# Performance work log

Hardware: AMD Instinct MI355X
Metric: run time of the kernel (lower is better)

The kernel has to match this reference:

```python
import jax, jax.numpy as jnp
import numpy as np

B, S, D, H, F = 8, 1024, 1024, 16, 4096
DH = D // H  # 64
EPS = 1e-12


def _layer_norm(x, g, b):
    mu = jnp.mean(x, axis=-1, keepdims=True)
    var = jnp.mean(jnp.square(x - mu), axis=-1, keepdims=True)
    return (x - mu) / jnp.sqrt(var + EPS) * g + b


def setup_inputs() -> dict:
    key = jax.random.key(0)
    ks = jax.random.split(key, 16)
    sd = 0.02
    inp = {
        "x": jax.random.normal(ks[0], (B, S, D), dtype=jnp.float32),
        "attn_mask": jnp.ones((B, S), dtype=jnp.int32),
        # attention projections (torch Linear: W is [out, in])
        "Wq": jax.random.normal(ks[1], (D, D), dtype=jnp.float32) * sd,
        "bq": jnp.zeros((D,), dtype=jnp.float32),
        "Wk": jax.random.normal(ks[2], (D, D), dtype=jnp.float32) * sd,
        "bk": jnp.zeros((D,), dtype=jnp.float32),
        "Wv": jax.random.normal(ks[3], (D, D), dtype=jnp.float32) * sd,
        "bv": jnp.zeros((D,), dtype=jnp.float32),
        "Wo": jax.random.normal(ks[4], (D, D), dtype=jnp.float32) * sd,
        "bo": jnp.zeros((D,), dtype=jnp.float32),
        # sa_layer_norm
        "ln1_g": jnp.ones((D,), dtype=jnp.float32),
        "ln1_b": jnp.zeros((D,), dtype=jnp.float32),
        # FFN
        "W1": jax.random.normal(ks[5], (F, D), dtype=jnp.float32) * sd,
        "b1": jnp.zeros((F,), dtype=jnp.float32),
        "W2": jax.random.normal(ks[6], (D, F), dtype=jnp.float32) * sd,
        "b2": jnp.zeros((D,), dtype=jnp.float32),
        # output_layer_norm
        "ln2_g": jnp.ones((D,), dtype=jnp.float32),
        "ln2_b": jnp.zeros((D,), dtype=jnp.float32),
    }
    return inp


def reference(x, attn_mask, Wq, bq, Wk, bk, Wv, bv, Wo, bo,
              ln1_g, ln1_b, W1, b1, W2, b2, ln2_g, ln2_b):
    b, s, d = x.shape

    def proj_heads(inp, W, bias):
        y = jnp.einsum('bsd,ed->bse', inp, W) + bias  # torch Linear: x @ W.T + b
        return y.reshape(b, s, H, DH).transpose(0, 2, 1, 3)  # (b, h, s, dh)

    q = proj_heads(x, Wq, bq) / jnp.sqrt(jnp.float32(DH))
    k = proj_heads(x, Wk, bk)
    v = proj_heads(x, Wv, bv)

    scores = jnp.einsum('bhqe,bhke->bhqk', q, k)  # (b, h, s, s)
    pad = (attn_mask == 0)[:, None, None, :]      # (b, 1, 1, s)
    scores = jnp.where(pad, -jnp.inf, scores)
    weights = jax.nn.softmax(scores, axis=-1)

    ctx = jnp.einsum('bhqk,bhke->bhqe', weights, v)
    ctx = ctx.transpose(0, 2, 1, 3).reshape(b, s, d)
    sa_out = jnp.einsum('bsd,ed->bse', ctx, Wo) + bo

    h = _layer_norm(sa_out + x, ln1_g, ln1_b)

    ff = jnp.einsum('bsd,fd->bsf', h, W1) + b1
    ff = jax.nn.gelu(ff, approximate=False)
    ff = jnp.einsum('bsf,df->bsd', ff, W2) + b2

    out = _layer_norm(ff + h, ln2_g, ln2_b)
    return out
```

## Files before the change

kernel.cpp:

```cpp
#include <hip/hip_runtime.h>
#include <math.h>

typedef __attribute__((ext_vector_type(8))) short short8;
typedef __attribute__((ext_vector_type(4))) float f32x4;

__device__ __forceinline__ unsigned short f2bf(float f) {
  unsigned int u = __float_as_uint(f);
  u += 0x7fffu + ((u >> 16) & 1u);
  return (unsigned short)(u >> 16);
}

__device__ __forceinline__ float gelu_f(float v) {
  float xa = fabsf(v) * 0.70710678118f;
  float t = __builtin_amdgcn_rcpf(1.f + 0.3275911f * xa);
  float p = t * (0.254829592f +
            t * (-0.284496736f +
            t * (1.421413741f +
            t * (-1.453152027f + t * 1.061405429f))));
  float erfa = 1.f - p * __expf(-xa * xa);
  return 0.5f * v * (1.f + copysignf(erfa, v));
}

__device__ __forceinline__ void gll16(const unsigned short* g, unsigned short* l) {
  __builtin_amdgcn_global_load_lds(
      (const __attribute__((address_space(1))) unsigned int*)(uintptr_t)g,
      (__attribute__((address_space(3))) unsigned int*)(uintptr_t)l, 16, 0, 0);
}

__global__ __launch_bounds__(256) void cvt_f32_bf16(const float* __restrict__ in,
                                                    unsigned short* __restrict__ out,
                                                    int n4) {
  int i = blockIdx.x * 256 + threadIdx.x;
  if (i >= n4) return;
  float4 f = reinterpret_cast<const float4*>(in)[i];
  ushort4 o;
  o.x = f2bf(f.x); o.y = f2bf(f.y); o.z = f2bf(f.z); o.w = f2bf(f.w);
  reinterpret_cast<ushort4*>(out)[i] = o;
}

__global__ __launch_bounds__(256) void cvt4_f32_bf16(
    const float* __restrict__ a, const float* __restrict__ b,
    const float* __restrict__ c, const float* __restrict__ d,
    unsigned short* __restrict__ oa, unsigned short* __restrict__ ob,
    unsigned short* __restrict__ oc, unsigned short* __restrict__ od) {
  const float* in = (blockIdx.y == 0) ? a : (blockIdx.y == 1) ? b : (blockIdx.y == 2) ? c : d;
  unsigned short* out = (blockIdx.y == 0) ? oa : (blockIdx.y == 1) ? ob : (blockIdx.y == 2) ? oc : od;
  int i = blockIdx.x * 256 + threadIdx.x;
  float4 f = reinterpret_cast<const float4*>(in)[i];
  ushort4 o;
  o.x = f2bf(f.x); o.y = f2bf(f.y); o.z = f2bf(f.z); o.w = f2bf(f.w);
  reinterpret_cast<ushort4*>(out)[i] = o;
}

template <int EPI, bool SWAP>
__global__ __launch_bounds__(256) void gemm_nt(
    const unsigned short* __restrict__ A, const unsigned short* __restrict__ B,
    const float* __restrict__ bias, const float* __restrict__ bias_k,
    int K, int N, const float* __restrict__ resid,
    unsigned short* __restrict__ outb, float* __restrict__ outf) {
  __shared__ __align__(16) unsigned short As[2][128 * 32];
  __shared__ __align__(16) unsigned short Bs[2][128 * 32];
  const int t = threadIdx.x;
  const int tm = blockIdx.y * 128, tn = blockIdx.x * 128;
  const int lane = t & 63, wv = t >> 6;
  const int wr = wv >> 1, wc = wv & 1;
  const int l15 = lane & 15, quad = lane >> 4;
  const int srow = lane >> 2;
  const int scol = (lane & 3) << 3;

  const unsigned short* pa0 = &A[(size_t)(tm + wv * 32 + srow) * K + scol];
  const unsigned short* pa1 = &A[(size_t)(tm + wv * 32 + 16 + srow) * K + scol];
  const unsigned short* pb0 = &B[(size_t)(tn + wv * 32 + srow) * K + scol];
  const unsigned short* pb1 = &B[(size_t)(tn + wv * 32 + 16 + srow) * K + scol];
  unsigned short* la0 = &As[0][(wv * 2) * 512];
  unsigned short* la1 = &As[0][(wv * 2 + 1) * 512];
  unsigned short* lb0 = &Bs[0][(wv * 2) * 512];
  unsigned short* lb1 = &Bs[0][(wv * 2 + 1) * 512];

  const f32x4 zero = {0.f, 0.f, 0.f, 0.f};
  f32x4 acc[4][4];
#pragma unroll
  for (int i = 0; i < 4; ++i)
#pragma unroll
    for (int j = 0; j < 4; ++j) acc[i][j] = zero;

  gll16(pa0, la0); pa0 += 32;
  gll16(pa1, la1); pa1 += 32;
  gll16(pb0, lb0); pb0 += 32;
  gll16(pb1, lb1); pb1 += 32;

  const int nIter = K >> 5;
  for (int it = 0; it < nIter; ++it) {
    __syncthreads();
    const int cur = (it & 1) * 4096;
    const int nxt = 4096 - cur;
    if (it + 1 < nIter) {
      gll16(pa0, la0 + nxt); pa0 += 32;
      gll16(pa1, la1 + nxt); pa1 += 32;
      gll16(pb0, lb0 + nxt); pb0 += 32;
      gll16(pb1, lb1 + nxt); pb1 += 32;
    }
    short8 af[4], bfr[4];
#pragma unroll
    for (int i = 0; i < 4; ++i) {
      af[i] = *reinterpret_cast<const short8*>(&As[0][cur + (wr * 64 + i * 16 + l15) * 32 + quad * 8]);
      bfr[i] = *reinterpret_cast<const short8*>(&Bs[0][cur + (wc * 64 + i * 16 + l15) * 32 + quad * 8]);
    }
#pragma unroll
    for (int i = 0; i < 4; ++i)
#pragma unroll
      for (int j = 0; j < 4; ++j)
        acc[i][j] = SWAP
            ? __builtin_amdgcn_mfma_f32_16x16x32_bf16(bfr[j], af[i], acc[i][j], 0, 0, 0)
            : __builtin_amdgcn_mfma_f32_16x16x32_bf16(af[i], bfr[j], acc[i][j], 0, 0, 0);
  }

  if (SWAP) {
#pragma unroll
    for (int i = 0; i < 4; ++i) {
      const int row = tm + wr * 64 + i * 16 + l15;
#pragma unroll
      for (int j = 0; j < 4; ++j) {
        const int col0 = tn + wc * 64 + j * 16 + quad * 4;
        if (EPI == 5) {
          const int chunk = col0 >> 10;
          const int colc = col0 & 1023;
          const float4 b4 = *reinterpret_cast<const float4*>(
              &(chunk == 0 ? bias : bias_k)[colc]);
          const float sc = (chunk == 0) ? 0.125f : 1.f;
          const int h = colc >> 6, dh = colc & 63;
          const int b = row >> 10, s = row & 1023;
          ushort4 pk;
          pk.x = f2bf((acc[i][j][0] + b4.x) * sc);
          pk.y = f2bf((acc[i][j][1] + b4.y) * sc);
          pk.z = f2bf((acc[i][j][2] + b4.z) * sc);
          pk.w = f2bf((acc[i][j][3] + b4.w) * sc);
          *reinterpret_cast<ushort4*>(
              &outb[((size_t)chunk << 23) + (((size_t)((b << 4) + h)) << 16) + (s << 6) + dh]) = pk;
        } else if (EPI == 2) {
          const float4 b4 = *reinterpret_cast<const float4*>(&bias[col0]);
          ushort4 pk;
          pk.x = f2bf(gelu_f(acc[i][j][0] + b4.x));
          pk.y = f2bf(gelu_f(acc[i][j][1] + b4.y));
          pk.z = f2bf(gelu_f(acc[i][j][2] + b4.z));
          pk.w = f2bf(gelu_f(acc[i][j][3] + b4.w));
          *reinterpret_cast<ushort4*>(&outb[(size_t)row * (size_t)N + col0]) = pk;
        } else {
          const float4 b4 = *reinterpret_cast<const float4*>(&bias[col0]);
          const size_t idx = (size_t)row * (size_t)N + col0;
          const float4 r4 = *reinterpret_cast<const float4*>(&resid[idx]);
          float4 o4;
          o4.x = acc[i][j][0] + b4.x + r4.x;
          o4.y = acc[i][j][1] + b4.y + r4.y;
          o4.z = acc[i][j][2] + b4.z + r4.z;
          o4.w = acc[i][j][3] + b4.w + r4.w;
          *reinterpret_cast<float4*>(&outf[idx]) = o4;
        }
      }
    }
  } else {
#pragma unroll
    for (int i = 0; i < 4; ++i) {
#pragma unroll
      for (int j = 0; j < 4; ++j) {
        const int col = tn + wc * 64 + j * 16 + l15;
        const float bcol = bias[col];
        const int h = col >> 6, dh = col & 63;
        const int row0 = tm + wr * 64 + i * 16 + quad * 4;
        const int b = row0 >> 10, s0 = row0 & 1023;
        ushort4 pk;
        pk.x = f2bf(acc[i][j][0] + bcol);
        pk.y = f2bf(acc[i][j][1] + bcol);
        pk.z = f2bf(acc[i][j][2] + bcol);
        pk.w = f2bf(acc[i][j][3] + bcol);
        *reinterpret_cast<ushort4*>(
            &outb[(((size_t)((b << 4) + h)) << 16) + (dh << 10) + s0]) = pk;
      }
    }
  }
}

__global__ __launch_bounds__(256) void attn_kernel(
    const unsigned short* __restrict__ Q, const unsigned short* __restrict__ Kc,
    const unsigned short* __restrict__ Vg, const int* __restrict__ mask,
    unsigned short* __restrict__ ctx) {
  __shared__ __align__(16) unsigned short Qs[64 * 64];
  __shared__ __align__(16) unsigned short Ks[2][64 * 64];
  __shared__ __align__(16) unsigned short Vs[2][64 * 64];
  __shared__ __align__(16) unsigned short Ps[4 * 16 * 72];
  __shared__ float maskf[1024];
  const int t = threadIdx.x;
  const int bh = blockIdx.x;
  const int qt = blockIdx.y;
  const int b = bh >> 4, h = bh & 15;
  const int lane = t & 63, wv = t >> 6, l15 = lane & 15, quad = lane >> 4;
  const int lr = lane >> 3;
  const int cs = (lane & 7) ^ lr;
  const unsigned short* Qp = Q + ((size_t)bh << 16);
  const unsigned short* Kp = Kc + ((size_t)bh << 16);
  const unsigned short* Vp = Vg + ((size_t)bh << 16);
  const int seg0 = wv * 2, seg1 = wv * 2 + 1;
  const int r0 = seg0 * 8 + lr, r1 = seg1 * 8 + lr;

  for (int i = t; i < 1024; i += 256)
    maskf[i] = mask[b * 1024 + i] ? -8.f : -INFINITY;
#pragma unroll
  for (int i = 0; i < 2; ++i) {
    const int seg = wv * 2 + i;
    gll16(&Qp[(qt * 64 + seg * 8 + lr) * 64 + cs * 8], &Qs[seg * 512]);
  }
  gll16(&Kp[r0 * 64 + cs * 8], &Ks[0][seg0 * 512]);
  gll16(&Kp[r1 * 64 + cs * 8], &Ks[0][seg1 * 512]);
  gll16(&Vp[r0 * 1024 + cs * 8], &Vs[0][seg0 * 512]);
  gll16(&Vp[r1 * 1024 + cs * 8], &Vs[0][seg1 * 512]);
  __syncthreads();
  const int sw0 = ((quad ^ (l15 & 7)) << 3);
  const int sw1 = (((quad + 4) ^ (l15 & 7)) << 3);
  const short8 qf0 = *reinterpret_cast<const short8*>(&Qs[(wv * 16 + l15) * 64 + sw0]);
  const short8 qf1 = *reinterpret_cast<const short8*>(&Qs[(wv * 16 + l15) * 64 + sw1]);

  const f32x4 zero = {0.f, 0.f, 0.f, 0.f};
  float ps[4] = {0.f, 0.f, 0.f, 0.f};
  f32x4 o[4];
#pragma unroll
  for (int j = 0; j < 4; ++j) o[j] = zero;

  unsigned short* Pw = &Ps[wv * 16 * 72];
  for (int kt = 0; kt < 16; ++kt) {
    const int cur = kt & 1;
    if (kt < 15) {
      const int nb = cur ^ 1;
      gll16(&Kp[((kt + 1) * 64 + r0) * 64 + cs * 8], &Ks[nb][seg0 * 512]);
      gll16(&Kp[((kt + 1) * 64 + r1) * 64 + cs * 8], &Ks[nb][seg1 * 512]);
      gll16(&Vp[r0 * 1024 + (kt + 1) * 64 + cs * 8], &Vs[nb][seg0 * 512]);
      gll16(&Vp[r1 * 1024 + (kt + 1) * 64 + cs * 8], &Vs[nb][seg1 * 512]);
    }

    f32x4 s4[4];
    float madd[4];
#pragma unroll
    for (int nt = 0; nt < 4; ++nt) {
      const int row = nt * 16 + l15;
      short8 kf0 = *reinterpret_cast<const short8*>(&Ks[cur][row * 64 + sw0]);
      short8 kf1 = *reinterpret_cast<const short8*>(&Ks[cur][row * 64 + sw1]);
      s4[nt] = __builtin_amdgcn_mfma_f32_16x16x32_bf16(qf0, kf0, zero, 0, 0, 0);
      s4[nt] = __builtin_amdgcn_mfma_f32_16x16x32_bf16(qf1, kf1, s4[nt], 0, 0, 0);
      madd[nt] = maskf[kt * 64 + nt * 16 + l15];
    }
#pragma unroll
    for (int nt = 0; nt < 4; ++nt) {
#pragma unroll
      for (int r = 0; r < 4; ++r) {
        float p = __expf(s4[nt][r] + madd[nt]);
        ps[r] += p;
        Pw[(quad * 4 + r) * 72 + nt * 16 + l15] = f2bf(p);
      }
    }
    short8 pf0 = *reinterpret_cast<const short8*>(&Pw[l15 * 72 + quad * 8]);
    short8 pf1 = *reinterpret_cast<const short8*>(&Pw[l15 * 72 + 32 + quad * 8]);
#pragma unroll
    for (int nt = 0; nt < 4; ++nt) {
      const int row = nt * 16 + l15;
      short8 vf0 = *reinterpret_cast<const short8*>(&Vs[cur][row * 64 + sw0]);
      short8 vf1 = *reinterpret_cast<const short8*>(&Vs[cur][row * 64 + sw1]);
      o[nt] = __builtin_amdgcn_mfma_f32_16x16x32_bf16(pf0, vf0, o[nt], 0, 0, 0);
      o[nt] = __builtin_amdgcn_mfma_f32_16x16x32_bf16(pf1, vf1, o[nt], 0, 0, 0);
    }
    __syncthreads();
  }

#pragma unroll
  for (int r = 0; r < 4; ++r) {
#pragma unroll
    for (int off = 8; off >= 1; off >>= 1) ps[r] += __shfl_xor(ps[r], off, 64);
  }
#pragma unroll
  for (int r = 0; r < 4; ++r) {
    float inv = 1.f / ps[r];
    int srow = qt * 64 + wv * 16 + quad * 4 + r;
#pragma unroll
    for (int nt = 0; nt < 4; ++nt) {
      int dh = nt * 16 + l15;
      ctx[((size_t)b << 20) + ((size_t)srow << 10) + (h << 6) + dh] = f2bf(o[nt][r] * inv);
    }
  }
}

__global__ __launch_bounds__(256) void ln_kernel(float* __restrict__ y,
                                                 const float* __restrict__ g,
                                                 const float* __restrict__ be,
                                                 unsigned short* __restrict__ hb) {
  __shared__ float sm[8];
  const int t = threadIdx.x;
  const size_t row = blockIdx.x;
  float* yr = y + (row << 10);
  float v[4];
#pragma unroll
  for (int i = 0; i < 4; ++i) v[i] = yr[t + (i << 8)];
  float s = v[0] + v[1] + v[2] + v[3];
#pragma unroll
  for (int off = 32; off >= 1; off >>= 1) s += __shfl_xor(s, off, 64);
  if ((t & 63) == 0) sm[t >> 6] = s;
  __syncthreads();
  float mu = (sm[0] + sm[1] + sm[2] + sm[3]) * (1.f / 1024.f);
  float q = 0.f;
#pragma unroll
  for (int i = 0; i < 4; ++i) { float d = v[i] - mu; q += d * d; }
#pragma unroll
  for (int off = 32; off >= 1; off >>= 1) q += __shfl_xor(q, off, 64);
  if ((t & 63) == 0) sm[4 + (t >> 6)] = q;
  __syncthreads();
  float var = (sm[4] + sm[5] + sm[6] + sm[7]) * (1.f / 1024.f);
  float rs = rsqrtf(var + 1e-12f);
#pragma unroll
  for (int i = 0; i < 4; ++i) {
    int c = t + (i << 8);
    float o = (v[i] - mu) * rs * g[c] + be[c];
    yr[c] = o;
    if (hb) hb[(row << 10) + c] = f2bf(o);
  }
}

extern "C" void kernel_launch(void* const* d_in, const int* in_sizes, int n_in,
                              void* d_out, int out_size, void* d_ws, size_t ws_size,
                              hipStream_t stream) {
  const float* x   = (const float*)d_in[0];
  const int*   msk = (const int*)d_in[1];
  const float* Wq  = (const float*)d_in[2];
  const float* bq  = (const float*)d_in[3];
  const float* Wk  = (const float*)d_in[4];
  const float* bk  = (const float*)d_in[5];
  const float* Wv  = (const float*)d_in[6];
  const float* bv  = (const float*)d_in[7];
  const float* Wo  = (const float*)d_in[8];
  const float* bo  = (const float*)d_in[9];
  const float* g1  = (const float*)d_in[10];
  const float* be1 = (const float*)d_in[11];
  const float* W1  = (const float*)d_in[12];
  const float* b1  = (const float*)d_in[13];
  const float* W2  = (const float*)d_in[14];
  const float* b2  = (const float*)d_in[15];
  const float* g2  = (const float*)d_in[16];
  const float* be2 = (const float*)d_in[17];
  float* out = (float*)d_out;

  unsigned short* Wqb = (unsigned short*)d_ws;
  unsigned short* Wkb = Wqb + (1u << 20);
  unsigned short* Wvb = Wkb + (1u << 20);
  unsigned short* Wob = Wvb + (1u << 20);
  unsigned short* W1b = Wob + (1u << 20);
  unsigned short* W2b = W1b + (4u << 20);
  unsigned short* xb  = W2b + (4u << 20);
  unsigned short* qb  = xb + (8u << 20);
  unsigned short* vb  = qb + (16u << 20);
  unsigned short* ctx = xb;
  unsigned short* ffb = xb;
  float* y1 = (float*)(qb + (24u << 20));
  unsigned short* hb = (unsigned short*)(y1 + (8u << 20));

  dim3 blk(256);
  cvt4_f32_bf16<<<dim3(1024, 4), blk, 0, stream>>>(Wq, Wk, Wv, Wo, Wqb, Wkb, Wvb, Wob);
  cvt_f32_bf16<<<dim3(4096), blk, 0, stream>>>(W1, W1b, 1 << 20);
  cvt_f32_bf16<<<dim3(4096), blk, 0, stream>>>(W2, W2b, 1 << 20);
  cvt_f32_bf16<<<dim3(8192), blk, 0, stream>>>(x, xb, 1 << 21);
  gemm_nt<5, true><<<dim3(16, 64), blk, 0, stream>>>(xb, Wqb, bq, bk, 1024, 1024,
                                                     nullptr, qb, nullptr);
  gemm_nt<4, false><<<dim3(8, 64), blk, 0, stream>>>(xb, Wvb, bv, nullptr, 1024, 1024,
                                                     nullptr, vb, nullptr);
  attn_kernel<<<dim3(128, 16), blk, 0, stream>>>(qb, qb + (8u << 20), vb, msk, ctx);
  gemm_nt<1, true><<<dim3(8, 64), blk, 0, stream>>>(ctx, Wob, bo, nullptr, 1024, 1024,
                                                    x, nullptr, y1);
  ln_kernel<<<dim3(8192), blk, 0, stream>>>(y1, g1, be1, hb);
  gemm_nt<2, true><<<dim3(32, 64), blk, 0, stream>>>(hb, W1b, b1, nullptr, 1024, 4096,
                                                     nullptr, ffb, nullptr);
  gemm_nt<1, true><<<dim3(8, 64), blk, 0, stream>>>(ffb, W2b, b2, nullptr, 4096, 1024,
                                                    y1, nullptr, out);
  ln_kernel<<<dim3(8192), blk, 0, stream>>>(out, g2, be2, nullptr);
}
```

Measured before the change: 568.5 us.

## Double attention query tile per block and merge weight conversion kernels

The attention kernel now processes 128 query rows per block, two 16-row groups per wave, so each K/V tile loaded into shared memory is reused twice. This halves the grid and the K/V traffic. Q fragments are loaded straight from global memory into registers, which removes the Q shared-memory staging and a barrier. The four fp32-to-bf16 conversion launches are merged into one kernel to cut launch overhead. The trade-off is more registers per wave and fewer blocks to hide latency.

```diff
diff --git a/kernel.cpp b/kernel.cpp
--- a/kernel.cpp
+++ b/kernel.cpp
@@ -27,25 +27,27 @@
       (__attribute__((address_space(3))) unsigned int*)(uintptr_t)l, 16, 0, 0);
 }
 
-__global__ __launch_bounds__(256) void cvt_f32_bf16(const float* __restrict__ in,
-                                                    unsigned short* __restrict__ out,
-                                                    int n4) {
-  int i = blockIdx.x * 256 + threadIdx.x;
-  if (i >= n4) return;
-  float4 f = reinterpret_cast<const float4*>(in)[i];
-  ushort4 o;
-  o.x = f2bf(f.x); o.y = f2bf(f.y); o.z = f2bf(f.z); o.w = f2bf(f.w);
-  reinterpret_cast<ushort4*>(out)[i] = o;
-}
-
-__global__ __launch_bounds__(256) void cvt4_f32_bf16(
-    const float* __restrict__ a, const float* __restrict__ b,
-    const float* __restrict__ c, const float* __restrict__ d,
-    unsigned short* __restrict__ oa, unsigned short* __restrict__ ob,
-    unsigned short* __restrict__ oc, unsigned short* __restrict__ od) {
-  const float* in = (blockIdx.y == 0) ? a : (blockIdx.y == 1) ? b : (blockIdx.y == 2) ? c : d;
-  unsigned short* out = (blockIdx.y == 0) ? oa : (blockIdx.y == 1) ? ob : (blockIdx.y == 2) ? oc : od;
-  int i = blockIdx.x * 256 + threadIdx.x;
+__global__ __launch_bounds__(256) void cvt_all(
+    const float* __restrict__ Wq, const float* __restrict__ Wk,
+    const float* __restrict__ Wv, const float* __restrict__ Wo,
+    const float* __restrict__ W1, const float* __restrict__ W2,
+    const float* __restrict__ x, unsigned short* __restrict__ ws) {
+  const int bi = blockIdx.x;
+  const float* in;
+  unsigned short* out;
+  int i;
+  if (bi < 4096) {
+    const int m = bi >> 10;
+    in = (m == 0) ? Wq : (m == 1) ? Wk : (m == 2) ? Wv : Wo;
+    out = ws + (size_t)m * (1u << 20);
+    i = (bi & 1023) * 256 + threadIdx.x;
+  } else if (bi < 8192) {
+    in = W1; out = ws + (4u << 20); i = (bi - 4096) * 256 + threadIdx.x;
+  } else if (bi < 12288) {
+    in = W2; out = ws + (8u << 20); i = (bi - 8192) * 256 + threadIdx.x;
+  } else {
+    in = x; out = ws + (12u << 20); i = (bi - 12288) * 256 + threadIdx.x;
+  }
   float4 f = reinterpret_cast<const float4*>(in)[i];
   ushort4 o;
   o.x = f2bf(f.x); o.y = f2bf(f.y); o.z = f2bf(f.z); o.w = f2bf(f.w);
@@ -184,10 +186,9 @@
     const unsigned short* __restrict__ Q, const unsigned short* __restrict__ Kc,
     const unsigned short* __restrict__ Vg, const int* __restrict__ mask,
     unsigned short* __restrict__ ctx) {
-  __shared__ __align__(16) unsigned short Qs[64 * 64];
   __shared__ __align__(16) unsigned short Ks[2][64 * 64];
   __shared__ __align__(16) unsigned short Vs[2][64 * 64];
-  __shared__ __align__(16) unsigned short Ps[4 * 16 * 72];
+  __shared__ __align__(16) unsigned short Ps[4][16 * 72];
   __shared__ float maskf[1024];
   const int t = threadIdx.x;
   const int bh = blockIdx.x;
@@ -204,29 +205,33 @@
 
   for (int i = t; i < 1024; i += 256)
     maskf[i] = mask[b * 1024 + i] ? -8.f : -INFINITY;
-#pragma unroll
-  for (int i = 0; i < 2; ++i) {
-    const int seg = wv * 2 + i;
-    gll16(&Qp[(qt * 64 + seg * 8 + lr) * 64 + cs * 8], &Qs[seg * 512]);
-  }
+
+  short8 qf[2][2];
+#pragma unroll
+  for (int g = 0; g < 2; ++g)
+#pragma unroll
+    for (int hh = 0; hh < 2; ++hh)
+      qf[g][hh] = *reinterpret_cast<const short8*>(
+          &Qp[(size_t)(qt * 128 + wv * 32 + g * 16 + l15) * 64 + hh * 32 + quad * 8]);
+
   gll16(&Kp[r0 * 64 + cs * 8], &Ks[0][seg0 * 512]);
   gll16(&Kp[r1 * 64 + cs * 8], &Ks[0][seg1 * 512]);
   gll16(&Vp[r0 * 1024 + cs * 8], &Vs[0][seg0 * 512]);
   gll16(&Vp[r1 * 1024 + cs * 8], &Vs[0][seg1 * 512]);
-  __syncthreads();
+
   const int sw0 = ((quad ^ (l15 & 7)) << 3);
   const int sw1 = (((quad + 4) ^ (l15 & 7)) << 3);
-  const short8 qf0 = *reinterpret_cast<const short8*>(&Qs[(wv * 16 + l15) * 64 + sw0]);
-  const short8 qf1 = *reinterpret_cast<const short8*>(&Qs[(wv * 16 + l15) * 64 + sw1]);
-
   const f32x4 zero = {0.f, 0.f, 0.f, 0.f};
-  float ps[4] = {0.f, 0.f, 0.f, 0.f};
-  f32x4 o[4];
-#pragma unroll
-  for (int j = 0; j < 4; ++j) o[j] = zero;
-
-  unsigned short* Pw = &Ps[wv * 16 * 72];
+  float ps[2][4];
+  f32x4 o[2][4];
+#pragma unroll
+  for (int g = 0; g < 2; ++g)
+#pragma unroll
+    for (int j = 0; j < 4; ++j) { o[g][j] = zero; ps[g][j] = 0.f; }
+
+  unsigned short* Pw = Ps[wv];
   for (int kt = 0; kt < 16; ++kt) {
+    __syncthreads();
     const int cur = kt & 1;
     if (kt < 15) {
       const int nb = cur ^ 1;
@@ -235,55 +240,61 @@
       gll16(&Vp[r0 * 1024 + (kt + 1) * 64 + cs * 8], &Vs[nb][seg0 * 512]);
       gll16(&Vp[r1 * 1024 + (kt + 1) * 64 + cs * 8], &Vs[nb][seg1 * 512]);
     }
-
-    f32x4 s4[4];
     float madd[4];
+    short8 kf[4][2];
 #pragma unroll
     for (int nt = 0; nt < 4; ++nt) {
-      const int row = nt * 16 + l15;
-      short8 kf0 = *reinterpret_cast<const short8*>(&Ks[cur][row * 64 + sw0]);
-      short8 kf1 = *reinterpret_cast<const short8*>(&Ks[cur][row * 64 + sw1]);
-      s4[nt] = __builtin_amdgcn_mfma_f32_16x16x32_bf16(qf0, kf0, zero, 0, 0, 0);
-      s4[nt] = __builtin_amdgcn_mfma_f32_16x16x32_bf16(qf1, kf1, s4[nt], 0, 0, 0);
+      const int row = (nt * 16 + l15) * 64;
+      kf[nt][0] = *reinterpret_cast<const short8*>(&Ks[cur][row + sw0]);
+      kf[nt][1] = *reinterpret_cast<const short8*>(&Ks[cur][row + sw1]);
       madd[nt] = maskf[kt * 64 + nt * 16 + l15];
     }
 #pragma unroll
-    for (int nt = 0; nt < 4; ++nt) {
-#pragma unroll
-      for (int r = 0; r < 4; ++r) {
-        float p = __expf(s4[nt][r] + madd[nt]);
-        ps[r] += p;
-        Pw[(quad * 4 + r) * 72 + nt * 16 + l15] = f2bf(p);
-      }
-    }
-    short8 pf0 = *reinterpret_cast<const short8*>(&Pw[l15 * 72 + quad * 8]);
-    short8 pf1 = *reinterpret_cast<const short8*>(&Pw[l15 * 72 + 32 + quad * 8]);
-#pragma unroll
-    for (int nt = 0; nt < 4; ++nt) {
-      const int row = nt * 16 + l15;
-      short8 vf0 = *reinterpret_cast<const short8*>(&Vs[cur][row * 64 + sw0]);
-      short8 vf1 = *reinterpret_cast<const short8*>(&Vs[cur][row * 64 + sw1]);
-      o[nt] = __builtin_amdgcn_mfma_f32_16x16x32_bf16(pf0, vf0, o[nt], 0, 0, 0);
-      o[nt] = __builtin_amdgcn_mfma_f32_16x16x32_bf16(pf1, vf1, o[nt], 0, 0, 0);
-    }
-    __syncthreads();
-  }
-
-#pragma unroll
-  for (int r = 0; r < 4; ++r) {
-#pragma unroll
-    for (int off = 8; off >= 1; off >>= 1) ps[r] += __shfl_xor(ps[r], off, 64);
-  }
-#pragma unroll
-  for (int r = 0; r < 4; ++r) {
-    float inv = 1.f / ps[r];
-    int srow = qt * 64 + wv * 16 + quad * 4 + r;
-#pragma unroll
-    for (int nt = 0; nt < 4; ++nt) {
-      int dh = nt * 16 + l15;
-      ctx[((size_t)b << 20) + ((size_t)srow << 10) + (h << 6) + dh] = f2bf(o[nt][r] * inv);
-    }
-  }
+    for (int g = 0; g < 2; ++g) {
+      f32x4 s4[4];
+#pragma unroll
+      for (int nt = 0; nt < 4; ++nt) {
+        s4[nt] = __builtin_amdgcn_mfma_f32_16x16x32_bf16(qf[g][0], kf[nt][0], zero, 0, 0, 0);
+        s4[nt] = __builtin_amdgcn_mfma_f32_16x16x32_bf16(qf[g][1], kf[nt][1], s4[nt], 0, 0, 0);
+      }
+#pragma unroll
+      for (int nt = 0; nt < 4; ++nt) {
+#pragma unroll
+        for (int r = 0; r < 4; ++r) {
+          float p = __expf(s4[nt][r] + madd[nt]);
+          ps[g][r] += p;
+          Pw[(quad * 4 + r) * 72 + nt * 16 + l15] = f2bf(p);
+        }
+      }
+      short8 pf0 = *reinterpret_cast<const short8*>(&Pw[l15 * 72 + quad * 8]);
+      short8 pf1 = *reinterpret_cast<const short8*>(&Pw[l15 * 72 + 32 + quad * 8]);
+#pragma unroll
+      for (int nt = 0; nt < 4; ++nt) {
+        const int row = (nt * 16 + l15) * 64;
+        short8 vf0 = *reinterpret_cast<const short8*>(&Vs[cur][row + sw0]);
+        short8 vf1 = *reinterpret_cast<const short8*>(&Vs[cur][row + sw1]);
+        o[g][nt] = __builtin_amdgcn_mfma_f32_16x16x32_bf16(pf0, vf0, o[g][nt], 0, 0, 0);
+        o[g][nt] = __builtin_amdgcn_mfma_f32_16x16x32_bf16(pf1, vf1, o[g][nt], 0, 0, 0);
+      }
+    }
+  }
+
+#pragma unroll
+  for (int g = 0; g < 2; ++g)
+#pragma unroll
+    for (int r = 0; r < 4; ++r) {
+      float v = ps[g][r];
+#pragma unroll
+      for (int off = 8; off >= 1; off >>= 1) v += __shfl_xor(v, off, 64);
+      const float inv = 1.f / v;
+      const int srow = qt * 128 + wv * 32 + g * 16 + quad * 4 + r;
+#pragma unroll
+      for (int nt = 0; nt < 4; ++nt) {
+        const int dh = nt * 16 + l15;
+        ctx[((size_t)b << 20) + ((size_t)srow << 10) + (h << 6) + dh] =
+            f2bf(o[g][nt][r] * inv);
+      }
+    }
 }
 
 __global__ __launch_bounds__(256) void ln_kernel(float* __restrict__ y,
@@ -345,8 +356,7 @@
   float* out = (float*)d_out;
 
   unsigned short* Wqb = (unsigned short*)d_ws;
-  unsigned short* Wkb = Wqb + (1u << 20);
-  unsigned short* Wvb = Wkb + (1u << 20);
+  unsigned short* Wvb = Wqb + (2u << 20);
   unsigned short* Wob = Wvb + (1u << 20);
   unsigned short* W1b = Wob + (1u << 20);
   unsigned short* W2b = W1b + (4u << 20);
@@ -359,15 +369,12 @@
   unsigned short* hb = (unsigned short*)(y1 + (8u << 20));
 
   dim3 blk(256);
-  cvt4_f32_bf16<<<dim3(1024, 4), blk, 0, stream>>>(Wq, Wk, Wv, Wo, Wqb, Wkb, Wvb, Wob);
-  cvt_f32_bf16<<<dim3(4096), blk, 0, stream>>>(W1, W1b, 1 << 20);
-  cvt_f32_bf16<<<dim3(4096), blk, 0, stream>>>(W2, W2b, 1 << 20);
-  cvt_f32_bf16<<<dim3(8192), blk, 0, stream>>>(x, xb, 1 << 21);
+  cvt_all<<<dim3(20480), blk, 0, stream>>>(Wq, Wk, Wv, Wo, W1, W2, x, (unsigned short*)d_ws);
   gemm_nt<5, true><<<dim3(16, 64), blk, 0, stream>>>(xb, Wqb, bq, bk, 1024, 1024,
                                                      nullptr, qb, nullptr);
   gemm_nt<4, false><<<dim3(8, 64), blk, 0, stream>>>(xb, Wvb, bv, nullptr, 1024, 1024,
                                                      nullptr, vb, nullptr);
-  attn_kernel<<<dim3(128, 16), blk, 0, stream>>>(qb, qb + (8u << 20), vb, msk, ctx);
+  attn_kernel<<<dim3(128, 8), blk, 0, stream>>>(qb, qb + (8u << 20), vb, msk, ctx);
   gemm_nt<1, true><<<dim3(8, 64), blk, 0, stream>>>(ctx, Wob, bo, nullptr, 1024, 1024,
                                                     x, nullptr, y1);
   ln_kernel<<<dim3(8192), blk, 0, stream>>>(y1, g1, be1, hb);
```

New measurement: 531.0 us. 1.07x faster.
